# Kernel tuning notes

Measured on AMD Instinct MI355X. Metric: run time of the kernel, lower is better.

The kernel has to match this reference:

```python
import jax, jax.numpy as jnp
import numpy as np

NUM_HEADS = 8
NUM_KV_HEADS = 4
HEAD_DIM = 256
HIDDEN = 2048
SEQ = 4096
CHUNK_START = 2048
CHUNK_END = 4096
SOFTCAP = 50.0
EPS = 1e-6
ROPE_THETA = 10000.0
NEG_INF = -1e9


def _rms_norm(x, w, eps=EPS):
    # Gemma RMSNorm: computed in fp32, scale is (1 + w)
    x32 = x.astype(jnp.float32)
    out = x32 * jax.lax.rsqrt(jnp.mean(x32 * x32, axis=-1, keepdims=True) + eps)
    return (out * (1.0 + w.astype(jnp.float32))).astype(x.dtype)


def _rotate_half(x):
    h = x.shape[-1] // 2
    return jnp.concatenate([-x[..., h:], x[..., :h]], axis=-1)


def _apply_rope(x, cos, sin):
    # x: [B, S, H, D]; cos/sin: [B, S, D] -> unsqueeze head dim
    cos = cos[:, :, None, :]
    sin = sin[:, :, None, :]
    return x * cos + _rotate_half(x) * sin


def setup_inputs() -> dict:
    key = jax.random.key(0)
    ks = jax.random.split(key, 8)
    hidden_states = jax.random.normal(ks[0], (1, SEQ, HIDDEN), dtype=jnp.float32)
    # real RoPE tables
    inv_freq = 1.0 / (ROPE_THETA ** (np.arange(0, HEAD_DIM, 2, dtype=np.float32) / HEAD_DIM))
    pos = np.arange(SEQ, dtype=np.float32)
    freqs = np.outer(pos, inv_freq)                      # [S, D/2]
    emb = np.concatenate([freqs, freqs], axis=-1)        # [S, D]
    cos = jnp.asarray(np.cos(emb))[None]                 # [1, S, D]
    sin = jnp.asarray(np.sin(emb))[None]
    # causal additive mask for the chunk: query i (abs pos start+i) attends keys j <= start+i
    q_pos = np.arange(CHUNK_START, CHUNK_END)[:, None]
    k_pos = np.arange(CHUNK_END)[None, :]
    attention_mask = jnp.asarray(np.where(k_pos <= q_pos, 0.0, NEG_INF).astype(np.float32))[None, None]
    s = 0.02
    wq = jax.random.normal(ks[1], (HIDDEN, NUM_HEADS * HEAD_DIM), dtype=jnp.float32) * s
    wk = jax.random.normal(ks[2], (HIDDEN, NUM_KV_HEADS * HEAD_DIM), dtype=jnp.float32) * s
    wv = jax.random.normal(ks[3], (HIDDEN, NUM_KV_HEADS * HEAD_DIM), dtype=jnp.float32) * s
    wo = jax.random.normal(ks[4], (NUM_HEADS * HEAD_DIM, HIDDEN), dtype=jnp.float32) * s
    q_norm_w = jnp.zeros((HEAD_DIM,), dtype=jnp.float32)
    k_norm_w = jnp.zeros((HEAD_DIM,), dtype=jnp.float32)
    v_norm_w = jnp.zeros((HEAD_DIM,), dtype=jnp.float32)
    return {
        'hidden_states': hidden_states, 'cos': cos, 'sin': sin,
        'attention_mask': attention_mask,
        'wq': wq, 'wk': wk, 'wv': wv, 'wo': wo,
        'q_norm_w': q_norm_w, 'k_norm_w': k_norm_w, 'v_norm_w': v_norm_w,
        'start': CHUNK_START, 'end': CHUNK_END,
    }


def reference(hidden_states, cos, sin, attention_mask, wq, wk, wv, wo,
              q_norm_w, k_norm_w, v_norm_w, start, end):
    B = hidden_states.shape[0]
    chunk = end - start
    scaling = HEAD_DIM ** -0.5

    # ---- queries from the chunk ----
    q = (hidden_states[:, start:end] @ wq).reshape(B, chunk, NUM_HEADS, HEAD_DIM)
    q = _rms_norm(q, q_norm_w)
    q = _apply_rope(q, cos[:, start:end], sin[:, start:end])
    q = q.transpose(0, 2, 1, 3)                         # [B, H, chunk, D]

    # ---- keys / values over [0, end) ----
    kv_h = hidden_states[:, :end]
    k = (kv_h @ wk).reshape(B, end, NUM_KV_HEADS, HEAD_DIM)
    k = _rms_norm(k, k_norm_w)
    k = _apply_rope(k, cos[:, :end], sin[:, :end]).transpose(0, 2, 1, 3)   # [B, KV, end, D]
    v = (kv_h @ wv).reshape(B, end, NUM_KV_HEADS, HEAD_DIM)
    v = _rms_norm(v, v_norm_w).transpose(0, 2, 1, 3)                        # [B, KV, end, D]

    # ---- GQA repeat_kv ----
    n_rep = NUM_HEADS // NUM_KV_HEADS
    k = jnp.repeat(k, n_rep, axis=1)                    # [B, H, end, D]
    v = jnp.repeat(v, n_rep, axis=1)

    # ---- eager attention with logit softcap ----
    logits = jnp.einsum('bhqd,bhkd->bhqk', q, k) * scaling
    logits = jnp.tanh(logits / SOFTCAP) * SOFTCAP
    logits = logits + attention_mask
    attn = jax.nn.softmax(logits.astype(jnp.float32), axis=-1).astype(q.dtype)
    out = jnp.einsum('bhqk,bhkd->bhqd', attn, v)
    out = out.transpose(0, 2, 1, 3).reshape(B, chunk, NUM_HEADS * HEAD_DIM)
    return out @ wo
```

## Files before the change

### kernel.cpp

```cpp
#include <hip/hip_runtime.h>

#define HID 2048
#define SEQL 4096
#define CHUNK 2048
#define NHEADS 8
#define NKVH 4
#define HDIM 256

typedef __bf16 bf16x4 __attribute__((ext_vector_type(4)));
typedef __bf16 bf16x8 __attribute__((ext_vector_type(8)));
typedef float f32x4 __attribute__((ext_vector_type(4)));
typedef _Float16 f16x4 __attribute__((ext_vector_type(4)));
typedef __attribute__((address_space(1))) unsigned int* as1_u32;
typedef __attribute__((address_space(3))) unsigned int* as3_u32;

__device__ __forceinline__ void load_lds16(const __bf16* g, __bf16* l) {
  __builtin_amdgcn_global_load_lds((as1_u32)g, (as3_u32)l, 16, 0, 0);
}

__global__ void prep_kernel(const float* __restrict__ X, __bf16* __restrict__ Y,
                            const float* __restrict__ wq, const float* __restrict__ wk,
                            const float* __restrict__ wv, const float* __restrict__ wo,
                            __bf16* __restrict__ WQT, __bf16* __restrict__ WKVT,
                            __bf16* __restrict__ WOT) {
  if (blockIdx.x < 8192) {
    int i = blockIdx.x * blockDim.x + threadIdx.x;
    const float4* xv = (const float4*)X;
    float4 v = xv[i];
    bf16x4 o;
    o[0] = (__bf16)v.x; o[1] = (__bf16)v.y; o[2] = (__bf16)v.z; o[3] = (__bf16)v.w;
    *(bf16x4*)(Y + i * 4) = o;
    return;
  }
  __shared__ float tile[64][65];
  const int b = blockIdx.x - 8192;
  const float* W;
  __bf16* WT;
  int R, C, bx, by;
  if (b < 1024) { W = wq; WT = WQT; R = 2048; C = 2048; bx = b & 31; by = b >> 5; }
  else if (b < 1536) { int q = b - 1024; W = wk; WT = WKVT; R = 2048; C = 1024; bx = q & 15; by = q >> 4; }
  else if (b < 2048) { int q = b - 1536; W = wv; WT = WKVT + (size_t)1024 * 2048; R = 2048; C = 1024; bx = q & 15; by = q >> 4; }
  else { int q = b - 2048; W = wo; WT = WOT; R = 2048; C = 2048; bx = q & 31; by = q >> 5; }
  int r0 = by * 64, c0 = bx * 64;
#pragma unroll
  for (int it = 0; it < 4; it++) {
    int idx = it * 256 + threadIdx.x;
    int r = idx >> 4, c4 = (idx & 15) * 4;
    float4 v = *(const float4*)&W[(size_t)(r0 + r) * C + c0 + c4];
    tile[r][c4] = v.x; tile[r][c4 + 1] = v.y; tile[r][c4 + 2] = v.z; tile[r][c4 + 3] = v.w;
  }
  __syncthreads();
#pragma unroll
  for (int it = 0; it < 2; it++) {
    int idx = it * 256 + threadIdx.x;
    int cc = idx >> 3, rb = (idx & 7) * 8;
    bf16x8 o;
#pragma unroll
    for (int j = 0; j < 8; j++) o[j] = (__bf16)tile[rb + j][cc];
    *(bf16x8*)&WT[(size_t)(c0 + cc) * R + r0 + rb] = o;
  }
}

template <int MODE>
__global__ __launch_bounds__(512, 2) void gemm256_kernel(
    const __bf16* __restrict__ A0, const __bf16* __restrict__ B0,
    const __bf16* __restrict__ B1, void* __restrict__ C0, void* __restrict__ C1) {
  __shared__ __bf16 Asm[2][256 * 64];
  __shared__ __bf16 Bsm[2][256 * 64];
  const int tid = threadIdx.x;
  const int lane = tid & 63, wave = tid >> 6;
  const int quad = lane >> 4, l15 = lane & 15;
  const int wm = (wave & 1) * 128, wn = (wave >> 1) * 64;

  const __bf16 *A, *B;
  char* Cb;
  int m0, n0;
  if (MODE == 0) {
    int b = blockIdx.x;
    if (b < 128) { A = A0; B = B0; Cb = (char*)C0; m0 = (b & 15) * 256; n0 = (b >> 4) * 256; }
    else { int q = b - 128; A = A0 + (size_t)2048 * 2048; B = B1; Cb = (char*)C1; m0 = (q & 7) * 256; n0 = (q >> 3) * 256; }
  } else {
    A = A0; B = B0; Cb = (char*)C0;
    m0 = (int)(blockIdx.x & 7) * 256; n0 = (int)(blockIdx.x >> 3) * 256;
  }

  f32x4 acc[8][4];
#pragma unroll
  for (int i = 0; i < 8; i++)
#pragma unroll
    for (int j = 0; j < 4; j++) acc[i][j] = (f32x4){0.f, 0.f, 0.f, 0.f};

  const int rr = tid >> 3;
  const int gch = (tid & 7) ^ ((tid >> 3) & 7);
  const int ldsb = wave * 512;

  const int sx = l15 & 7;
  const int s0 = ((0 + quad) ^ sx) * 8;
  const int s1 = ((4 + quad) ^ sx) * 8;

#define STAGE(T, BF)                                                                  \
  {                                                                                   \
    const int k0s = (T) * 64;                                                         \
    _Pragma("unroll")                                                                 \
    for (int a = 0; a < 4; a++) {                                                     \
      load_lds16(A + (size_t)(m0 + a * 64 + rr) * 2048 + k0s + gch * 8,               \
                 &Asm[BF][a * 4096 + ldsb]);                                          \
      load_lds16(B + (size_t)(n0 + a * 64 + rr) * 2048 + k0s + gch * 8,               \
                 &Bsm[BF][a * 4096 + ldsb]);                                          \
    }                                                                                 \
  }

#define LDA(MH, BF)                                                                   \
  _Pragma("unroll")                                                                   \
  for (int mi = 0; mi < 4; mi++) {                                                    \
    const int rowb = (wm + (MH) * 64 + mi * 16 + l15) * 64;                           \
    af[mi * 2 + 0] = *(const bf16x8*)(&Asm[BF][rowb + s0]);                           \
    af[mi * 2 + 1] = *(const bf16x8*)(&Asm[BF][rowb + s1]);                           \
  }

#define LDB(DST, NH, BF)                                                              \
  _Pragma("unroll")                                                                   \
  for (int ni = 0; ni < 2; ni++) {                                                    \
    const int rowb = (wn + (NH) * 32 + ni * 16 + l15) * 64;                           \
    DST[ni * 2 + 0] = *(const bf16x8*)(&Bsm[BF][rowb + s0]);                          \
    DST[ni * 2 + 1] = *(const bf16x8*)(&Bsm[BF][rowb + s1]);                          \
  }

#define MMA(MH, NH, BV)                                                               \
  _Pragma("unroll")                                                                   \
  for (int mi = 0; mi < 4; mi++)                                                      \
    _Pragma("unroll")                                                                 \
    for (int ni = 0; ni < 2; ni++) {                                                  \
      acc[(MH) * 4 + mi][(NH) * 2 + ni] = __builtin_amdgcn_mfma_f32_16x16x32_bf16(    \
          af[mi * 2 + 0], BV[ni * 2 + 0], acc[(MH) * 4 + mi][(NH) * 2 + ni], 0, 0, 0);\
      acc[(MH) * 4 + mi][(NH) * 2 + ni] = __builtin_amdgcn_mfma_f32_16x16x32_bf16(    \
          af[mi * 2 + 1], BV[ni * 2 + 1], acc[(MH) * 4 + mi][(NH) * 2 + ni], 0, 0, 0);\
    }

  bf16x8 af[8], bX[4], bY[4];

  STAGE(0, 0);
  STAGE(1, 1);
  asm volatile("s_waitcnt vmcnt(8)" ::: "memory");
  __builtin_amdgcn_s_barrier();

  const int NT = 32;
#pragma unroll 2
  for (int t = 0; t < NT; t++) {
    const int c = t & 1;
    LDA(0, c);
    LDB(bX, 0, c);
    LDB(bY, 1, c);
    MMA(0, 0, bX);
    MMA(0, 1, bY);
    LDA(1, c);
    MMA(1, 1, bY);
    MMA(1, 0, bX);
    __builtin_amdgcn_s_barrier();
    if (t + 2 < NT) {
      STAGE(t + 2, c);
      asm volatile("s_waitcnt vmcnt(8)" ::: "memory");
      __builtin_amdgcn_s_barrier();
    } else if (t + 1 < NT) {
      asm volatile("s_waitcnt vmcnt(0)" ::: "memory");
      __builtin_amdgcn_s_barrier();
    }
  }

#pragma unroll
  for (int mh = 0; mh < 2; mh++)
#pragma unroll
    for (int mi = 0; mi < 4; mi++) {
      const int r = m0 + wm + mh * 64 + mi * 16 + quad * 4;
#pragma unroll
      for (int ni = 0; ni < 4; ni++) {
        const int cc = n0 + wn + (ni >> 1) * 32 + (ni & 1) * 16 + l15;
#pragma unroll
        for (int j = 0; j < 4; j++) {
          if (MODE == 1)
            ((float*)Cb)[(size_t)(r + j) * 2048 + cc] = acc[mh * 4 + mi][ni][j];
          else
            ((__bf16*)Cb)[(size_t)(r + j) * 2048 + cc] = (__bf16)acc[mh * 4 + mi][ni][j];
        }
      }
    }
#undef STAGE
#undef LDA
#undef LDB
#undef MMA
}

template <int NI, bool F32OUT>
__global__ __launch_bounds__(256, 2) void gemm_bt_kernel(
    const __bf16* __restrict__ A, const __bf16* __restrict__ B,
    void* __restrict__ Cv, int M, int N, int Kd) {
  constexpr int BN = NI * 32;
  __shared__ __bf16 Asm[2][128 * 32];
  __shared__ __bf16 Bsm[2][BN * 32];
  const int tid = threadIdx.x;
  const int lane = tid & 63, wave = tid >> 6;
  const int quad = lane >> 4, l15 = lane & 15;
  const int m0 = blockIdx.x * 128, n0 = blockIdx.y * BN;
  const int wm = (wave & 1) * 64, wn = (wave >> 1) * (NI * 16);
  f32x4 acc[4][NI];
#pragma unroll
  for (int i = 0; i < 4; i++)
#pragma unroll
    for (int j = 0; j < NI; j++) acc[i][j] = (f32x4){0.f, 0.f, 0.f, 0.f};

  const int rA = lane >> 2, cA = (lane & 3) * 8;

#pragma unroll
  for (int c = wave; c < 8; c += 4)
    load_lds16(A + (size_t)(m0 + c * 16 + rA) * Kd + cA, &Asm[0][c * 512]);
#pragma unroll
  for (int c = wave; c < BN / 16; c += 4)
    load_lds16(B + (size_t)(n0 + c * 16 + rA) * Kd + cA, &Bsm[0][c * 512]);

  for (int k0 = 0; k0 < Kd; k0 += 32) {
    const int buf = (k0 >> 5) & 1;
    __syncthreads();
    if (k0 + 32 < Kd) {
#pragma unroll
      for (int c = wave; c < 8; c += 4)
        load_lds16(A + (size_t)(m0 + c * 16 + rA) * Kd + k0 + 32 + cA, &Asm[buf ^ 1][c * 512]);
#pragma unroll
      for (int c = wave; c < BN / 16; c += 4)
        load_lds16(B + (size_t)(n0 + c * 16 + rA) * Kd + k0 + 32 + cA, &Bsm[buf ^ 1][c * 512]);
    }
    bf16x8 af[4], bfr[NI];
#pragma unroll
    for (int i = 0; i < 4; i++)
      af[i] = *(const bf16x8*)(&Asm[buf][(wm + i * 16 + l15) * 32 + quad * 8]);
#pragma unroll
    for (int i = 0; i < NI; i++)
      bfr[i] = *(const bf16x8*)(&Bsm[buf][(wn + i * 16 + l15) * 32 + quad * 8]);
#pragma unroll
    for (int mi = 0; mi < 4; mi++)
#pragma unroll
      for (int ni = 0; ni < NI; ni++)
        acc[mi][ni] = __builtin_amdgcn_mfma_f32_16x16x32_bf16(af[mi], bfr[ni], acc[mi][ni], 0, 0, 0);
  }
#pragma unroll
  for (int mi = 0; mi < 4; mi++) {
    int r = m0 + wm + mi * 16 + quad * 4;
#pragma unroll
    for (int ni = 0; ni < NI; ni++) {
      int cc = n0 + wn + ni * 16 + l15;
#pragma unroll
      for (int j = 0; j < 4; j++) {
        if (F32OUT)
          ((float*)Cv)[(size_t)(r + j) * N + cc] = acc[mi][ni][j];
        else
          ((__bf16*)Cv)[(size_t)(r + j) * N + cc] = (__bf16)acc[mi][ni][j];
      }
    }
  }
}

__global__ void norm_all_kernel(__bf16* __restrict__ Qp, __bf16* __restrict__ KVp,
                                const float* __restrict__ cosb, const float* __restrict__ sinb,
                                const float* __restrict__ qw, const float* __restrict__ kw,
                                const float* __restrict__ vw) {
  const int gw = (blockIdx.x * 256 + threadIdx.x) >> 6;
  const int lane = threadIdx.x & 63;
  const int d0 = lane * 4;

  __bf16* row;
  const float* w;
  int pos = -1;
  bool isV = false;
  float prescale = 1.f;
  if (gw < 16384) {
    int t = gw >> 3, h = gw & 7;
    row = Qp + (size_t)t * 2048 + h * 256;
    w = qw; pos = t + 2048; prescale = 0.0625f;
  } else {
    int g2 = gw - 16384;
    int t = g2 >> 3, r = g2 & 7;
    if (r < 4) {
      row = KVp + (size_t)t * 2048 + r * 256;
      w = kw; pos = t;
    } else {
      row = KVp + (size_t)t * 2048 + 1024 + (r - 4) * 256;
      w = vw; isV = true;
    }
  }

  bf16x4 rv = *(const bf16x4*)(row + d0);
  float x[4];
  float ss = 0.f;
#pragma unroll
  for (int j = 0; j < 4; j++) { x[j] = (float)rv[j]; ss += x[j] * x[j]; }
#pragma unroll
  for (int off = 1; off < 64; off <<= 1) ss += __shfl_xor(ss, off);
  float scale = rsqrtf(ss * (1.f / 256.f) + 1e-6f);
  float n[4];
#pragma unroll
  for (int j = 0; j < 4; j++) n[j] = x[j] * scale * (1.f + w[d0 + j]);

  if (!isV) {
    const float* cp = cosb + (size_t)pos * 256 + d0;
    const float* sp = sinb + (size_t)pos * 256 + d0;
    bf16x4 ov;
#pragma unroll
    for (int j = 0; j < 4; j++) {
      float other = __shfl_xor(n[j], 32);
      float rot = (lane < 32) ? -other : other;
      ov[j] = (__bf16)((n[j] * cp[j] + rot * sp[j]) * prescale);
    }
    *(bf16x4*)(row + d0) = ov;
  } else {
    bf16x4 ov;
#pragma unroll
    for (int j = 0; j < 4; j++) ov[j] = (__bf16)n[j];
    *(bf16x4*)(row + d0) = ov;
  }
}

__global__ void vtrans_kernel(const __bf16* __restrict__ KVp, __bf16* __restrict__ VT) {
  __shared__ __bf16 tile[64][72];
  const int b = blockIdx.x;
  const int h = b >> 8;
  const int r = b & 255;
  const int t0 = (r >> 2) * 64;
  const int d0 = (r & 3) * 64;
  const __bf16* src = KVp + 1024 + h * 256 + d0;
#pragma unroll
  for (int it = 0; it < 2; it++) {
    int idx = it * 256 + threadIdx.x;
    int tt = idx >> 3, dd = (idx & 7) * 8;
    *(bf16x8*)(&tile[tt][dd]) = *(const bf16x8*)(src + (size_t)(t0 + tt) * 2048 + dd);
  }
  __syncthreads();
  __bf16* dst = VT + (size_t)h * (256 * 4096) + (size_t)d0 * 4096 + t0;
#pragma unroll
  for (int it = 0; it < 2; it++) {
    int idx = it * 256 + threadIdx.x;
    int dd = idx >> 3, tt = (idx & 7) * 8;
    bf16x8 o;
#pragma unroll
    for (int j = 0; j < 8; j++) o[j] = tile[tt + j][dd];
    *(bf16x8*)(dst + (size_t)dd * 4096 + tt) = o;
  }
}

__global__ __launch_bounds__(256, 2) void attn_kernel(
    const __bf16* __restrict__ Q,
    const __bf16* __restrict__ K,
    const __bf16* __restrict__ VT,
    _Float16* __restrict__ Op,
    float* __restrict__ Lp) {
  __shared__ __bf16 Ksm[2][8][32][32];
  __shared__ __bf16 Vsm[2][256][32];
  __shared__ __bf16 Pex[4][32][40];
  const int tid = threadIdx.x;
  const int lane = tid & 63, wave = tid >> 6;
  const int quad = lane >> 4, l15 = lane & 15;
  const int b = blockIdx.x;
  const int idx = b & 255;
  const int h = idx & 7, sp = (idx >> 3) & 3;
  int qt = idx >> 5;
  if (b >= 256) qt = 15 - qt;
  const int kvh = h >> 1;

  const int T = 68 + 4 * qt;
  const int nst = T >> 2;

  bf16x8 qf[2][8];
#pragma unroll
  for (int r = 0; r < 2; r++) {
    const __bf16* qp = Q + (size_t)(qt * 128 + wave * 32 + r * 16 + l15) * 2048 + h * 256 + quad * 8;
#pragma unroll
    for (int s = 0; s < 8; s++) qf[r][s] = *(const bf16x8*)(qp + s * 32);
  }
  f32x4 o[2][16];
#pragma unroll
  for (int r = 0; r < 2; r++)
#pragma unroll
    for (int i = 0; i < 16; i++) o[r][i] = (f32x4){0.f, 0.f, 0.f, 0.f};
  float rs[2][4] = {{0.f, 0.f, 0.f, 0.f}, {0.f, 0.f, 0.f, 0.f}};

  const __bf16* Kb = K + kvh * 256;
  const __bf16* Vb = VT + (size_t)kvh * (256 * 4096);
  const int rA = lane >> 2;
  const int cAs = (((lane & 3) ^ ((rA >> 1) & 3)) * 8);
  const int kx = (quad ^ ((l15 >> 1) & 3)) * 8;
  const int qbase = 2048 + qt * 128 + wave * 32 + quad * 4;

  {
    const int t0 = sp * 32;
#pragma unroll
    for (int ch = 0; ch < 4; ch++) {
      int cc = wave + ch * 4;
      int s = cc >> 1, hf = cc & 1;
      load_lds16(Kb + (size_t)(t0 + hf * 16 + rA) * 2048 + s * 32 + cAs, &Ksm[0][s][hf * 16][0]);
      load_lds16(Vb + (size_t)(cc * 16 + rA) * 4096 + t0 + cAs, &Vsm[0][cc * 16][0]);
    }
  }

  for (int i = 0; i < nst; i++) {
    const int buf = i & 1;
    const int t0 = (4 * i + sp) * 32;
    __syncthreads();
    if (i + 1 < nst) {
      const int t1 = t0 + 128;
#pragma unroll
      for (int ch = 0; ch < 4; ch++) {
        int cc = wave + ch * 4;
        int s = cc >> 1, hf = cc & 1;
        load_lds16(Kb + (size_t)(t1 + hf * 16 + rA) * 2048 + s * 32 + cAs, &Ksm[buf ^ 1][s][hf * 16][0]);
        load_lds16(Vb + (size_t)(cc * 16 + rA) * 4096 + t1 + cAs, &Vsm[buf ^ 1][cc * 16][0]);
      }
    }

    f32x4 s4[2][2];
    s4[0][0] = (f32x4){0.f, 0.f, 0.f, 0.f};
    s4[0][1] = s4[0][0]; s4[1][0] = s4[0][0]; s4[1][1] = s4[0][0];
#pragma unroll
    for (int s = 0; s < 8; s++) {
      bf16x8 b0 = *(const bf16x8*)(&Ksm[buf][s][l15][kx]);
      bf16x8 b1 = *(const bf16x8*)(&Ksm[buf][s][16 + l15][kx]);
      s4[0][0] = __builtin_amdgcn_mfma_f32_16x16x32_bf16(qf[0][s], b0, s4[0][0], 0, 0, 0);
      s4[0][1] = __builtin_amdgcn_mfma_f32_16x16x32_bf16(qf[0][s], b1, s4[0][1], 0, 0, 0);
      s4[1][0] = __builtin_amdgcn_mfma_f32_16x16x32_bf16(qf[1][s], b0, s4[1][0], 0, 0, 0);
      s4[1][1] = __builtin_amdgcn_mfma_f32_16x16x32_bf16(qf[1][s], b1, s4[1][1], 0, 0, 0);
    }

    const bool mk = (i == nst - 1);
#pragma unroll
    for (int r = 0; r < 2; r++)
#pragma unroll
      for (int nt = 0; nt < 2; nt++) {
        const int key = t0 + nt * 16 + l15;
#pragma unroll
        for (int j = 0; j < 4; j++) {
          float v = s4[r][nt][j];
          float e = __expf(v * 0.04f);
          float p = __expf(-100.f * __builtin_amdgcn_rcpf(e + 1.f));
          if (mk && key > qbase + r * 16 + j) p = 0.f;
          s4[r][nt][j] = p;
          rs[r][j] += p;
        }
      }

#pragma unroll
    for (int r = 0; r < 2; r++)
#pragma unroll
      for (int nt = 0; nt < 2; nt++)
#pragma unroll
        for (int j = 0; j < 4; j++)
          Pex[wave][r * 16 + quad * 4 + j][nt * 16 + l15] = (__bf16)s4[r][nt][j];

    bf16x8 pf0 = *(const bf16x8*)(&Pex[wave][l15][quad * 8]);
    bf16x8 pf1 = *(const bf16x8*)(&Pex[wave][16 + l15][quad * 8]);
#pragma unroll
    for (int d = 0; d < 16; d++) {
      bf16x8 vf = *(const bf16x8*)(&Vsm[buf][d * 16 + l15][kx]);
      o[0][d] = __builtin_amdgcn_mfma_f32_16x16x32_bf16(pf0, vf, o[0][d], 0, 0, 0);
      o[1][d] = __builtin_amdgcn_mfma_f32_16x16x32_bf16(pf1, vf, o[1][d], 0, 0, 0);
    }
  }

#pragma unroll
  for (int off = 1; off < 16; off <<= 1)
#pragma unroll
    for (int r = 0; r < 2; r++)
#pragma unroll
      for (int j = 0; j < 4; j++) rs[r][j] += __shfl_xor(rs[r][j], off);

  _Float16* Os = Op + (size_t)sp * (2048 * 2048);
  float* Ls = Lp + sp * (2048 * 8);
#pragma unroll
  for (int r = 0; r < 2; r++) {
    float inv[4];
#pragma unroll
    for (int j = 0; j < 4; j++)
      inv[j] = rs[r][j] > 0.f ? 1.f / rs[r][j] : 0.f;
    const int trow = qt * 128 + wave * 32 + r * 16 + quad * 4;
#pragma unroll
    for (int d = 0; d < 16; d++) {
      const int col = h * 256 + d * 16 + l15;
#pragma unroll
      for (int j = 0; j < 4; j++)
        Os[(size_t)(trow + j) * 2048 + col] = (_Float16)(o[r][d][j] * inv[j]);
    }
    if (l15 == 0) {
#pragma unroll
      for (int j = 0; j < 4; j++) Ls[(trow + j) * 8 + h] = rs[r][j];
    }
  }
}

__global__ void merge_kernel(const _Float16* __restrict__ Op, const float* __restrict__ Lp,
                             __bf16* __restrict__ AO) {
  int f = (blockIdx.x * 256 + threadIdx.x) * 4;
  int q = f >> 11, col = f & 2047, h = col >> 8;
  float lsum = 0.f;
  float acc[4] = {0.f, 0.f, 0.f, 0.f};
#pragma unroll
  for (int s = 0; s < 4; s++) {
    float l = Lp[s * (2048 * 8) + q * 8 + h];
    lsum += l;
    f16x4 v = *(const f16x4*)(Op + (size_t)s * (2048 * 2048) + f);
#pragma unroll
    for (int j = 0; j < 4; j++) acc[j] += l * (float)v[j];
  }
  float inv = 1.f / lsum;
  bf16x4 o;
#pragma unroll
  for (int j = 0; j < 4; j++) o[j] = (__bf16)(acc[j] * inv);
  *(bf16x4*)(AO + f) = o;
}

extern "C" void kernel_launch(void* const* d_in, const int* in_sizes, int n_in,
                              void* d_out, int out_size, void* d_ws, size_t ws_size,
                              hipStream_t stream) {
  const float* hidden = (const float*)d_in[0];
  const float* cosb = (const float*)d_in[1];
  const float* sinb = (const float*)d_in[2];
  const float* wq = (const float*)d_in[4];
  const float* wk = (const float*)d_in[5];
  const float* wv = (const float*)d_in[6];
  const float* wo = (const float*)d_in[7];
  const float* qw = (const float*)d_in[8];
  const float* kw = (const float*)d_in[9];
  const float* vw = (const float*)d_in[10];
  float* outp = (float*)d_out;

  char* p = (char*)d_ws;
  __bf16* Xb = (__bf16*)p;   p += (size_t)SEQL * HID * 2;
  __bf16* WQT = (__bf16*)p;  p += (size_t)2048 * 2048 * 2;
  __bf16* WKVT = (__bf16*)p; p += (size_t)2048 * 2048 * 2;
  __bf16* WOT = (__bf16*)p;  p += (size_t)2048 * 2048 * 2;
  __bf16* Qp = (__bf16*)p;   p += (size_t)2048 * 2048 * 2;
  __bf16* KVp = (__bf16*)p;  p += (size_t)4096 * 2048 * 2;
  __bf16* VT = (__bf16*)p;   p += (size_t)4 * 256 * 4096 * 2;
  __bf16* AO = (__bf16*)p;   p += (size_t)2048 * 2048 * 2;
  float* Lpart = (float*)p;  p += (size_t)4 * 2048 * 8 * 4;
  _Float16* Opart = (_Float16*)Xb;

  prep_kernel<<<11264, 256, 0, stream>>>(hidden, Xb, wq, wk, wv, wo, WQT, WKVT, WOT);

  gemm256_kernel<0><<<192, 512, 0, stream>>>(Xb, WKVT, WQT, KVp, Qp);

  norm_all_kernel<<<12288, 256, 0, stream>>>(Qp, KVp, cosb, sinb, qw, kw, vw);
  vtrans_kernel<<<1024, 256, 0, stream>>>(KVp, VT);

  attn_kernel<<<512, 256, 0, stream>>>(Qp, KVp, VT, Opart, Lpart);
  merge_kernel<<<4096, 256, 0, stream>>>(Opart, Lpart, AO);

  gemm_bt_kernel<4, true><<<dim3(16, 16), 256, 0, stream>>>(AO, WOT, outp, 2048, 2048, 2048);
}
```

Before: 361.8 us.

## Replace full syncthreads with partial vmcnt waits to deepen GEMM and attention prefetch

The GEMM main loop is restructured so that the loads for tile t+2 are issued into the buffer just consumed, after a barrier. It then waits only until the previous stage's loads complete (vmcnt(4)), so a global-to-LDS copy stays in flight across each compute step. The attention loop likewise swaps __syncthreads for a raw barrier with an explicit vmcnt(8) wait that leaves the next stage's loads outstanding. The goal is to overlap memory latency with MFMA work instead of draining every load at each barrier. The hardcoded vmcnt literals depend on exact per-thread load counts, enforced by a static_assert for NI==4, so any compiler reordering or shape change could produce LDS races.

```diff
diff --git a/kernel.cpp b/kernel.cpp
--- a/kernel.cpp
+++ b/kernel.cpp
@@ -195,6 +195,7 @@
     const __bf16* __restrict__ A, const __bf16* __restrict__ B,
     void* __restrict__ Cv, int M, int N, int Kd) {
   constexpr int BN = NI * 32;
+  static_assert(NI == 4, "vmcnt literals assume 4 loads/thread per stage");
   __shared__ __bf16 Asm[2][128 * 32];
   __shared__ __bf16 Bsm[2][BN * 32];
   const int tid = threadIdx.x;
@@ -216,18 +217,18 @@
 #pragma unroll
   for (int c = wave; c < BN / 16; c += 4)
     load_lds16(B + (size_t)(n0 + c * 16 + rA) * Kd + cA, &Bsm[0][c * 512]);
-
-  for (int k0 = 0; k0 < Kd; k0 += 32) {
-    const int buf = (k0 >> 5) & 1;
-    __syncthreads();
-    if (k0 + 32 < Kd) {
-#pragma unroll
-      for (int c = wave; c < 8; c += 4)
-        load_lds16(A + (size_t)(m0 + c * 16 + rA) * Kd + k0 + 32 + cA, &Asm[buf ^ 1][c * 512]);
-#pragma unroll
-      for (int c = wave; c < BN / 16; c += 4)
-        load_lds16(B + (size_t)(n0 + c * 16 + rA) * Kd + k0 + 32 + cA, &Bsm[buf ^ 1][c * 512]);
-    }
+#pragma unroll
+  for (int c = wave; c < 8; c += 4)
+    load_lds16(A + (size_t)(m0 + c * 16 + rA) * Kd + 32 + cA, &Asm[1][c * 512]);
+#pragma unroll
+  for (int c = wave; c < BN / 16; c += 4)
+    load_lds16(B + (size_t)(n0 + c * 16 + rA) * Kd + 32 + cA, &Bsm[1][c * 512]);
+  asm volatile("s_waitcnt vmcnt(4)" ::: "memory");
+  __builtin_amdgcn_s_barrier();
+
+  const int NT = Kd >> 5;
+  for (int t = 0; t < NT; t++) {
+    const int buf = t & 1;
     bf16x8 af[4], bfr[NI];
 #pragma unroll
     for (int i = 0; i < 4; i++)
@@ -240,6 +241,21 @@
 #pragma unroll
       for (int ni = 0; ni < NI; ni++)
         acc[mi][ni] = __builtin_amdgcn_mfma_f32_16x16x32_bf16(af[mi], bfr[ni], acc[mi][ni], 0, 0, 0);
+    __builtin_amdgcn_s_barrier();
+    if (t + 2 < NT) {
+      const int kn = (t + 2) * 32;
+#pragma unroll
+      for (int c = wave; c < 8; c += 4)
+        load_lds16(A + (size_t)(m0 + c * 16 + rA) * Kd + kn + cA, &Asm[buf][c * 512]);
+#pragma unroll
+      for (int c = wave; c < BN / 16; c += 4)
+        load_lds16(B + (size_t)(n0 + c * 16 + rA) * Kd + kn + cA, &Bsm[buf][c * 512]);
+      asm volatile("s_waitcnt vmcnt(4)" ::: "memory");
+      __builtin_amdgcn_s_barrier();
+    } else if (t + 1 < NT) {
+      asm volatile("s_waitcnt vmcnt(0)" ::: "memory");
+      __builtin_amdgcn_s_barrier();
+    }
   }
 #pragma unroll
   for (int mi = 0; mi < 4; mi++) {
@@ -402,7 +418,7 @@
   for (int i = 0; i < nst; i++) {
     const int buf = i & 1;
     const int t0 = (4 * i + sp) * 32;
-    __syncthreads();
+    __builtin_amdgcn_s_barrier();
     if (i + 1 < nst) {
       const int t1 = t0 + 128;
 #pragma unroll
@@ -412,7 +428,11 @@
         load_lds16(Kb + (size_t)(t1 + hf * 16 + rA) * 2048 + s * 32 + cAs, &Ksm[buf ^ 1][s][hf * 16][0]);
         load_lds16(Vb + (size_t)(cc * 16 + rA) * 4096 + t1 + cAs, &Vsm[buf ^ 1][cc * 16][0]);
       }
-    }
+      asm volatile("s_waitcnt vmcnt(8)" ::: "memory");
+    } else {
+      asm volatile("s_waitcnt vmcnt(0)" ::: "memory");
+    }
+    __builtin_amdgcn_s_barrier();
 
     f32x4 s4[2][2];
     s4[0][0] = (f32x4){0.f, 0.f, 0.f, 0.f};
```

Result: no change. 355.5 us (-1.7%).
